# Performance work log

Measured on AMD Instinct MI355X. Metric: run time of the kernel, lower is better.

Reference implementation:

```python
import jax, jax.numpy as jnp
import numpy as np

F = 64      # input_v_size
E = 64      # emb_v_size
H = 8       # int(sqrt(emb_v_size))
P = 512     # proj_e_size
B, T = 64, 256


def setup_inputs() -> dict:
    key = jax.random.key(0)
    ks = jax.random.split(key, 14)
    s1 = 1.0            # Linear(1->H): fan_in=1
    s2 = 1.0 / np.sqrt(H)
    s3 = 1.0 / np.sqrt(F * E)
    return {
        "x":    jax.random.normal(ks[0], (B, T, F), dtype=jnp.float32),
        "time": jax.random.uniform(ks[1], (B, T, F), dtype=jnp.float32),
        # stacked per-feature Linear(1->H): weight [F,H], bias [F,H]
        "w1v": jax.random.uniform(ks[2], (F, H), jnp.float32, -s1, s1),
        "b1v": jax.random.uniform(ks[3], (F, H), jnp.float32, -s1, s1),
        # stacked per-feature Linear(H->E, bias=False): [F,H,E]
        "w2v": jax.random.uniform(ks[4], (F, H, E), jnp.float32, -s2, s2),
        "w1t": jax.random.uniform(ks[5], (F, H), jnp.float32, -s1, s1),
        "b1t": jax.random.uniform(ks[6], (F, H), jnp.float32, -s1, s1),
        "w2t": jax.random.uniform(ks[7], (F, H, E), jnp.float32, -s2, s2),
        # Wx, Wt: Linear(F*E -> P) stored as [F*E, P] (= torch weight.T)
        "wx":  jax.random.uniform(ks[8], (F * E, P), jnp.float32, -s3, s3),
        "bx":  jax.random.uniform(ks[9], (P,), jnp.float32, -s3, s3),
        "wt":  jax.random.uniform(ks[10], (F * E, P), jnp.float32, -s3, s3),
        "bt":  jax.random.uniform(ks[11], (P,), jnp.float32, -s3, s3),
    }


def _branch(inp, w1, b1, w2):
    # inp [B,T,F]; w1,b1 [F,H]; w2 [F,H,E]
    h = jnp.tanh(inp[..., None] * w1 + b1)          # [B,T,F,H]
    e = jnp.einsum("btfh,fhe->btfe", h, w2)          # [B,T,F,E]
    return e.reshape(*inp.shape[:2], -1)              # [B,T,F*E]


def reference(x, time, w1v, b1v, w2v, w1t, b1t, w2t, wx, bx, wt, bt):
    x_out = _branch(x, w1v, b1v, w2v)
    t_out = _branch(time, w1t, b1t, w2t)
    return (x_out @ wx + bx) + (t_out @ wt + bt)      # [B,T,P]
```

## Files before the change

### kernel.cpp

```cpp
#include <hip/hip_runtime.h>
#include <cstdint>
#include <cstddef>

#define FF 64
#define EE 64
#define HH 8
#define PP 512
#define MM 16384
#define KK 1024

typedef __bf16 bf16x8 __attribute__((ext_vector_type(8)));
typedef float  floatx4 __attribute__((ext_vector_type(4)));

__device__ __forceinline__ unsigned short f2bf(float f) {
    unsigned int u = __float_as_uint(f);
    u += 0x7FFFu + ((u >> 16) & 1u);
    return (unsigned short)(u >> 16);
}

__device__ __forceinline__ unsigned pack2(unsigned short a, unsigned short b) {
    return (unsigned)a | ((unsigned)b << 16);
}

__device__ __forceinline__ float fast_tanh(float x) {
    float e, r;
    asm("v_exp_f32 %0, %1" : "=v"(e) : "v"(x * 2.8853900817779268f));
    float d = e + 1.0f;
    asm("v_rcp_f32 %0, %1" : "=v"(r) : "v"(d));
    return __builtin_fmaf(-2.0f, r, 1.0f);
}

__device__ __forceinline__ void gl_lds16(const unsigned short* g, unsigned short* s) {
    __builtin_amdgcn_global_load_lds(
        (__attribute__((address_space(1))) void*)(void*)g,
        (__attribute__((address_space(3))) void*)s,
        16, 0, 0);
}

__global__ __launch_bounds__(256) void prep_kernel(
    const float* __restrict__ x,   const float* __restrict__ tmv,
    const float* __restrict__ w1v, const float* __restrict__ b1v,
    const float* __restrict__ w1t, const float* __restrict__ b1t,
    const float* __restrict__ w2v, const float* __restrict__ w2t,
    const float* __restrict__ wx,  const float* __restrict__ wt,
    unsigned short* __restrict__ BmatT, unsigned short* __restrict__ Hc)
{
    const int tid = threadIdx.x;
    if (blockIdx.x < 256) {
        const int bid = blockIdx.x;
        const int br = bid >> 7;
        const int f  = (bid >> 1) & 63;
        const int nh = bid & 1;
        const float* __restrict__ w2 = br ? w2t : w2v;
        const float* __restrict__ W  = br ? wt  : wx;
        __shared__ float w2s[HH * EE];
        for (int i = tid; i < HH * EE; i += 256) w2s[i] = w2[f * HH * EE + i];
        __syncthreads();
        const int n = nh * 256 + tid;
        float acc[HH] = {0,0,0,0,0,0,0,0};
        const float* Wcol = W + (size_t)f * EE * PP + n;
        #pragma unroll 8
        for (int e = 0; e < EE; ++e) {
            const float wv = Wcol[(size_t)e * PP];
            #pragma unroll
            for (int h = 0; h < HH; ++h)
                acc[h] = __builtin_fmaf(w2s[h * EE + e], wv, acc[h]);
        }
        uint4 v;
        v.x = pack2(f2bf(acc[0]), f2bf(acc[1]));
        v.y = pack2(f2bf(acc[2]), f2bf(acc[3]));
        v.z = pack2(f2bf(acc[4]), f2bf(acc[5]));
        v.w = pack2(f2bf(acc[6]), f2bf(acc[7]));
        *reinterpret_cast<uint4*>(&BmatT[(size_t)n * KK + br * 512 + f * 8]) = v;
    } else {
        const int g   = (blockIdx.x - 256) * 256 + tid;
        const int row = g >> 7;
        const int j   = g & 127;
        const int br  = j >> 6;
        const int f   = j & 63;
        const float val = br ? tmv[(size_t)row * FF + f] : x[(size_t)row * FF + f];
        const float* w1 = br ? w1t : w1v;
        const float* b1 = br ? b1t : b1v;
        const float4 wa = reinterpret_cast<const float4*>(w1)[f * 2];
        const float4 wb = reinterpret_cast<const float4*>(w1)[f * 2 + 1];
        const float4 ba = reinterpret_cast<const float4*>(b1)[f * 2];
        const float4 bb = reinterpret_cast<const float4*>(b1)[f * 2 + 1];
        float hv[8];
        hv[0] = fast_tanh(__builtin_fmaf(val, wa.x, ba.x));
        hv[1] = fast_tanh(__builtin_fmaf(val, wa.y, ba.y));
        hv[2] = fast_tanh(__builtin_fmaf(val, wa.z, ba.z));
        hv[3] = fast_tanh(__builtin_fmaf(val, wa.w, ba.w));
        hv[4] = fast_tanh(__builtin_fmaf(val, wb.x, bb.x));
        hv[5] = fast_tanh(__builtin_fmaf(val, wb.y, bb.y));
        hv[6] = fast_tanh(__builtin_fmaf(val, wb.z, bb.z));
        hv[7] = fast_tanh(__builtin_fmaf(val, wb.w, bb.w));
        uint4 v;
        v.x = pack2(f2bf(hv[0]), f2bf(hv[1]));
        v.y = pack2(f2bf(hv[2]), f2bf(hv[3]));
        v.z = pack2(f2bf(hv[4]), f2bf(hv[5]));
        v.w = pack2(f2bf(hv[6]), f2bf(hv[7]));
        *reinterpret_cast<uint4*>(&Hc[(size_t)row * KK + br * 512 + f * 8]) = v;
    }
}

__global__ __launch_bounds__(256) void gemm_kernel(
    const unsigned short* __restrict__ A,
    const unsigned short* __restrict__ Bt,
    const float* __restrict__ bx, const float* __restrict__ bt,
    float* __restrict__ out)
{
    __shared__ unsigned short As[128 * 64];
    __shared__ unsigned short Bs[128 * 64];
    const int tid  = threadIdx.x;
    const int wave = tid >> 6;
    const int lane = tid & 63;
    const int m0 = blockIdx.x * 128;
    const int n0 = blockIdx.y * 128;
    const int wr = wave >> 1;
    const int wc = wave & 1;
    const int q   = lane >> 4;
    const int ml  = lane & 15;
    const int mlx = ml & 7;
    const int lr  = lane >> 3;
    const int lkg = ((lane & 7) ^ lr) * 8;

    floatx4 acc[4][4];
    #pragma unroll
    for (int i = 0; i < 4; ++i)
        #pragma unroll
        for (int j = 0; j < 4; ++j)
            acc[i][j] = (floatx4){0.f, 0.f, 0.f, 0.f};

    for (int k0 = 0; k0 < KK; k0 += 64) {
        #pragma unroll
        for (int i = 0; i < 4; ++i) {
            const int seg = wave * 4 + i;
            const int r = seg * 8 + lr;
            gl_lds16(&A [(size_t)(m0 + r) * KK + k0 + lkg], &As[seg * 512]);
            gl_lds16(&Bt[(size_t)(n0 + r) * KK + k0 + lkg], &Bs[seg * 512]);
        }
        __syncthreads();
        #pragma unroll
        for (int kk = 0; kk < 64; kk += 32) {
            const int cl = (kk >> 3) + q;
            const int co = (cl ^ mlx) * 8;
            bf16x8 af[4], bfr[4];
            #pragma unroll
            for (int mt = 0; mt < 4; ++mt)
                af[mt] = *reinterpret_cast<const bf16x8*>(
                    &As[(wr * 64 + mt * 16 + ml) * 64 + co]);
            #pragma unroll
            for (int nt = 0; nt < 4; ++nt)
                bfr[nt] = *reinterpret_cast<const bf16x8*>(
                    &Bs[(wc * 64 + nt * 16 + ml) * 64 + co]);
            #pragma unroll
            for (int mt = 0; mt < 4; ++mt)
                #pragma unroll
                for (int nt = 0; nt < 4; ++nt)
                    acc[mt][nt] = __builtin_amdgcn_mfma_f32_16x16x32_bf16(
                        af[mt], bfr[nt], acc[mt][nt], 0, 0, 0);
        }
        __syncthreads();
    }

    #pragma unroll
    for (int nt = 0; nt < 4; ++nt) {
        const int n = n0 + wc * 64 + nt * 16 + ml;
        const float bias = bx[n] + bt[n];
        #pragma unroll
        for (int mt = 0; mt < 4; ++mt) {
            const int mb = m0 + wr * 64 + mt * 16 + q * 4;
            #pragma unroll
            for (int r = 0; r < 4; ++r)
                out[(size_t)(mb + r) * PP + n] = acc[mt][nt][r] + bias;
        }
    }
}

extern "C" void kernel_launch(void* const* d_in, const int* in_sizes, int n_in,
                              void* d_out, int out_size, void* d_ws, size_t ws_size,
                              hipStream_t stream)
{
    const float* x   = (const float*)d_in[0];
    const float* tmv = (const float*)d_in[1];
    const float* w1v = (const float*)d_in[2];
    const float* b1v = (const float*)d_in[3];
    const float* w2v = (const float*)d_in[4];
    const float* w1t = (const float*)d_in[5];
    const float* b1t = (const float*)d_in[6];
    const float* w2t = (const float*)d_in[7];
    const float* wx  = (const float*)d_in[8];
    const float* bx  = (const float*)d_in[9];
    const float* wt  = (const float*)d_in[10];
    const float* bt  = (const float*)d_in[11];
    float* out = (float*)d_out;

    unsigned short* Bws = (unsigned short*)d_ws;
    unsigned short* Hws = (unsigned short*)((char*)d_ws + (1u << 20));

    prep_kernel<<<256 + MM * KK / 8 / 256, 256, 0, stream>>>(
        x, tmv, w1v, b1v, w1t, b1t, w2v, w2t, wx, wt, Bws, Hws);
    gemm_kernel<<<dim3(MM / 128, PP / 128), 256, 0, stream>>>(Hws, Bws, bx, bt, out);
}
```

Before: 127.3 us.

## Fuse tanh hidden-feature computation into GEMM A-tile loading

Moves the per-feature Linear+tanh step that built the bf16 A matrix (32 MB) out of the prep kernel and into the GEMM: each block computes its A tile directly into LDS from x/time and cached w1/b1. This removes the write and re-read of the intermediate activation buffer through global memory. The price is that the tanh work is redone by each of the 4 column blocks, and the A tile is no longer loaded asynchronously.

```diff
diff --git a/kernel.cpp b/kernel.cpp
--- a/kernel.cpp
+++ b/kernel.cpp
@@ -37,85 +37,68 @@
         16, 0, 0);
 }
 
-__global__ __launch_bounds__(256) void prep_kernel(
+__global__ __launch_bounds__(256) void combine_kernel(
+    const float* __restrict__ w2v, const float* __restrict__ w2t,
+    const float* __restrict__ wx,  const float* __restrict__ wt,
+    unsigned short* __restrict__ BmatT)
+{
+    const int tid = threadIdx.x;
+    const int bid = blockIdx.x;
+    const int br = bid >> 7;
+    const int f  = (bid >> 1) & 63;
+    const int nh = bid & 1;
+    const float* __restrict__ w2 = br ? w2t : w2v;
+    const float* __restrict__ W  = br ? wt  : wx;
+    __shared__ float w2s[HH * EE];
+    for (int i = tid; i < HH * EE; i += 256) w2s[i] = w2[f * HH * EE + i];
+    __syncthreads();
+    const int n = nh * 256 + tid;
+    float acc[HH] = {0,0,0,0,0,0,0,0};
+    const float* Wcol = W + (size_t)f * EE * PP + n;
+    #pragma unroll 8
+    for (int e = 0; e < EE; ++e) {
+        const float wv = Wcol[(size_t)e * PP];
+        #pragma unroll
+        for (int h = 0; h < HH; ++h)
+            acc[h] = __builtin_fmaf(w2s[h * EE + e], wv, acc[h]);
+    }
+    uint4 v;
+    v.x = pack2(f2bf(acc[0]), f2bf(acc[1]));
+    v.y = pack2(f2bf(acc[2]), f2bf(acc[3]));
+    v.z = pack2(f2bf(acc[4]), f2bf(acc[5]));
+    v.w = pack2(f2bf(acc[6]), f2bf(acc[7]));
+    *reinterpret_cast<uint4*>(&BmatT[(size_t)n * KK + br * 512 + f * 8]) = v;
+}
+
+__global__ __launch_bounds__(256) void gemm_fused_kernel(
     const float* __restrict__ x,   const float* __restrict__ tmv,
     const float* __restrict__ w1v, const float* __restrict__ b1v,
     const float* __restrict__ w1t, const float* __restrict__ b1t,
-    const float* __restrict__ w2v, const float* __restrict__ w2t,
-    const float* __restrict__ wx,  const float* __restrict__ wt,
-    unsigned short* __restrict__ BmatT, unsigned short* __restrict__ Hc)
-{
-    const int tid = threadIdx.x;
-    if (blockIdx.x < 256) {
-        const int bid = blockIdx.x;
-        const int br = bid >> 7;
-        const int f  = (bid >> 1) & 63;
-        const int nh = bid & 1;
-        const float* __restrict__ w2 = br ? w2t : w2v;
-        const float* __restrict__ W  = br ? wt  : wx;
-        __shared__ float w2s[HH * EE];
-        for (int i = tid; i < HH * EE; i += 256) w2s[i] = w2[f * HH * EE + i];
-        __syncthreads();
-        const int n = nh * 256 + tid;
-        float acc[HH] = {0,0,0,0,0,0,0,0};
-        const float* Wcol = W + (size_t)f * EE * PP + n;
-        #pragma unroll 8
-        for (int e = 0; e < EE; ++e) {
-            const float wv = Wcol[(size_t)e * PP];
-            #pragma unroll
-            for (int h = 0; h < HH; ++h)
-                acc[h] = __builtin_fmaf(w2s[h * EE + e], wv, acc[h]);
-        }
-        uint4 v;
-        v.x = pack2(f2bf(acc[0]), f2bf(acc[1]));
-        v.y = pack2(f2bf(acc[2]), f2bf(acc[3]));
-        v.z = pack2(f2bf(acc[4]), f2bf(acc[5]));
-        v.w = pack2(f2bf(acc[6]), f2bf(acc[7]));
-        *reinterpret_cast<uint4*>(&BmatT[(size_t)n * KK + br * 512 + f * 8]) = v;
-    } else {
-        const int g   = (blockIdx.x - 256) * 256 + tid;
-        const int row = g >> 7;
-        const int j   = g & 127;
-        const int br  = j >> 6;
-        const int f   = j & 63;
-        const float val = br ? tmv[(size_t)row * FF + f] : x[(size_t)row * FF + f];
-        const float* w1 = br ? w1t : w1v;
-        const float* b1 = br ? b1t : b1v;
-        const float4 wa = reinterpret_cast<const float4*>(w1)[f * 2];
-        const float4 wb = reinterpret_cast<const float4*>(w1)[f * 2 + 1];
-        const float4 ba = reinterpret_cast<const float4*>(b1)[f * 2];
-        const float4 bb = reinterpret_cast<const float4*>(b1)[f * 2 + 1];
-        float hv[8];
-        hv[0] = fast_tanh(__builtin_fmaf(val, wa.x, ba.x));
-        hv[1] = fast_tanh(__builtin_fmaf(val, wa.y, ba.y));
-        hv[2] = fast_tanh(__builtin_fmaf(val, wa.z, ba.z));
-        hv[3] = fast_tanh(__builtin_fmaf(val, wa.w, ba.w));
-        hv[4] = fast_tanh(__builtin_fmaf(val, wb.x, bb.x));
-        hv[5] = fast_tanh(__builtin_fmaf(val, wb.y, bb.y));
-        hv[6] = fast_tanh(__builtin_fmaf(val, wb.z, bb.z));
-        hv[7] = fast_tanh(__builtin_fmaf(val, wb.w, bb.w));
-        uint4 v;
-        v.x = pack2(f2bf(hv[0]), f2bf(hv[1]));
-        v.y = pack2(f2bf(hv[2]), f2bf(hv[3]));
-        v.z = pack2(f2bf(hv[4]), f2bf(hv[5]));
-        v.w = pack2(f2bf(hv[6]), f2bf(hv[7]));
-        *reinterpret_cast<uint4*>(&Hc[(size_t)row * KK + br * 512 + f * 8]) = v;
-    }
-}
-
-__global__ __launch_bounds__(256) void gemm_kernel(
-    const unsigned short* __restrict__ A,
     const unsigned short* __restrict__ Bt,
     const float* __restrict__ bx, const float* __restrict__ bt,
     float* __restrict__ out)
 {
-    __shared__ unsigned short As[128 * 64];
-    __shared__ unsigned short Bs[128 * 64];
+    __shared__ __align__(16) unsigned short As[128 * 64];
+    __shared__ __align__(16) unsigned short Bs[128 * 64];
+    __shared__ __align__(16) float w1s[2 * FF * HH];
+    __shared__ __align__(16) float b1s[2 * FF * HH];
+
     const int tid  = threadIdx.x;
     const int wave = tid >> 6;
     const int lane = tid & 63;
     const int m0 = blockIdx.x * 128;
     const int n0 = blockIdx.y * 128;
+
+    {
+        const float4 wsrc = (tid < 128) ? reinterpret_cast<const float4*>(w1v)[tid]
+                                        : reinterpret_cast<const float4*>(w1t)[tid - 128];
+        const float4 bsrc = (tid < 128) ? reinterpret_cast<const float4*>(b1v)[tid]
+                                        : reinterpret_cast<const float4*>(b1t)[tid - 128];
+        reinterpret_cast<float4*>(w1s)[tid] = wsrc;
+        reinterpret_cast<float4*>(b1s)[tid] = bsrc;
+    }
+    __syncthreads();
+
     const int wr = wave >> 1;
     const int wc = wave & 1;
     const int q   = lane >> 4;
@@ -123,6 +106,8 @@
     const int mlx = ml & 7;
     const int lr  = lane >> 3;
     const int lkg = ((lane & 7) ^ lr) * 8;
+    const int fi  = tid & 7;
+    const int g   = tid >> 3;
 
     floatx4 acc[4][4];
     #pragma unroll
@@ -132,14 +117,50 @@
             acc[i][j] = (floatx4){0.f, 0.f, 0.f, 0.f};
 
     for (int k0 = 0; k0 < KK; k0 += 64) {
+        const int br = k0 >> 9;
+        const int f0 = (k0 >> 3) & 63;
+
         #pragma unroll
         for (int i = 0; i < 4; ++i) {
             const int seg = wave * 4 + i;
-            const int r = seg * 8 + lr;
-            gl_lds16(&A [(size_t)(m0 + r) * KK + k0 + lkg], &As[seg * 512]);
-            gl_lds16(&Bt[(size_t)(n0 + r) * KK + k0 + lkg], &Bs[seg * 512]);
+            gl_lds16(&Bt[(size_t)(n0 + seg * 8 + lr) * KK + k0 + lkg], &Bs[seg * 512]);
+        }
+
+        {
+            const float* __restrict__ inp = br ? tmv : x;
+            const int f = f0 + fi;
+            const float4 wlo = reinterpret_cast<const float4*>(w1s)[br * 128 + f * 2];
+            const float4 whi = reinterpret_cast<const float4*>(w1s)[br * 128 + f * 2 + 1];
+            const float4 blo = reinterpret_cast<const float4*>(b1s)[br * 128 + f * 2];
+            const float4 bhi = reinterpret_cast<const float4*>(b1s)[br * 128 + f * 2 + 1];
+            float vals[4];
+            #pragma unroll
+            for (int j = 0; j < 4; ++j)
+                vals[j] = inp[(size_t)(m0 + g + 32 * j) * FF + f];
+            const int pchunk = (fi ^ (g & 7)) * 8;
+            #pragma unroll
+            for (int j = 0; j < 4; ++j) {
+                const int r = g + 32 * j;
+                const float val = vals[j];
+                float hv[8];
+                hv[0] = fast_tanh(__builtin_fmaf(val, wlo.x, blo.x));
+                hv[1] = fast_tanh(__builtin_fmaf(val, wlo.y, blo.y));
+                hv[2] = fast_tanh(__builtin_fmaf(val, wlo.z, blo.z));
+                hv[3] = fast_tanh(__builtin_fmaf(val, wlo.w, blo.w));
+                hv[4] = fast_tanh(__builtin_fmaf(val, whi.x, bhi.x));
+                hv[5] = fast_tanh(__builtin_fmaf(val, whi.y, bhi.y));
+                hv[6] = fast_tanh(__builtin_fmaf(val, whi.z, bhi.z));
+                hv[7] = fast_tanh(__builtin_fmaf(val, whi.w, bhi.w));
+                uint4 v;
+                v.x = pack2(f2bf(hv[0]), f2bf(hv[1]));
+                v.y = pack2(f2bf(hv[2]), f2bf(hv[3]));
+                v.z = pack2(f2bf(hv[4]), f2bf(hv[5]));
+                v.w = pack2(f2bf(hv[6]), f2bf(hv[7]));
+                *reinterpret_cast<uint4*>(&As[r * 64 + pchunk]) = v;
+            }
         }
         __syncthreads();
+
         #pragma unroll
         for (int kk = 0; kk < 64; kk += 32) {
             const int cl = (kk >> 3) + q;
@@ -196,9 +217,8 @@
     float* out = (float*)d_out;
 
     unsigned short* Bws = (unsigned short*)d_ws;
-    unsigned short* Hws = (unsigned short*)((char*)d_ws + (1u << 20));
-
-    prep_kernel<<<256 + MM * KK / 8 / 256, 256, 0, stream>>>(
-        x, tmv, w1v, b1v, w1t, b1t, w2v, w2t, wx, wt, Bws, Hws);
-    gemm_kernel<<<dim3(MM / 128, PP / 128), 256, 0, stream>>>(Hws, Bws, bx, bt, out);
-}
+
+    combine_kernel<<<256, 256, 0, stream>>>(w2v, w2t, wx, wt, Bws);
+    gemm_fused_kernel<<<dim3(MM / 128, PP / 128), 256, 0, stream>>>(
+        x, tmv, w1v, b1v, w1t, b1t, Bws, bx, bt, out);
+}
```

Result: slower. 141.7 us (+11.3%).
